# Kernel optimization log

Hardware: AMD Instinct MI355X
Metric: run time of the kernel (lower is better)

The kernel has to match this reference:

```python
import jax, jax.numpy as jnp
import numpy as np

B, N, M, K, H = 32, 2048, 16, 32, 2
EPS = 1e-7


def setup_inputs() -> dict:
    key = jax.random.key(0)
    k1, k2, k3, k4, k5 = jax.random.split(key, 5)
    coords = jax.random.normal(k1, (B, N, M), jnp.float32)
    hom = jax.random.randint(k2, (B, N), 0, H).astype(jnp.float32)
    # ragged lengths: valid points first, all-zero padding rows after
    lengths = jax.random.randint(k3, (B,), N // 2, N + 1)
    rowmask = (jnp.arange(N)[None, :] < lengths[:, None]).astype(jnp.float32)
    dgm = jnp.concatenate([hom[..., None], coords], axis=-1) * rowmask[..., None]
    # tf.random_normal_initializer default stddev = 0.05
    theta = 0.05 * jax.random.normal(k4, (K, M), jnp.float32)
    class_w = 0.05 * jax.random.normal(k5, (H,), jnp.float32)
    return {"dgm": dgm, "theta": theta, "class_w": class_w}


def reference(dgm, theta, class_w):
    # dgm: [B, N, M+1]; dgm[:,:,0] = homology class, rest = point coords
    b, n = dgm.shape[0], dgm.shape[1]
    k, m = theta.shape
    hom = jnp.clip(dgm[:, :, 0].astype(jnp.int32), 0, class_w.shape[0] - 1)  # [B,N]
    y = dgm[:, :, 1:]                                                        # [B,N,m]
    # while-loop semantics: process points until the FIRST all-zero row
    nonzero = jnp.any(dgm != 0, axis=-1)
    valid = jnp.cumprod(nonzero.astype(dgm.dtype), axis=1)                   # [B,N]
    w = class_w[hom] * valid                                                 # [B,N]
    # Poincare parametrization: z = theta_k * y, map R^m -> ball via z/(1+sqrt(1+|z|^2))
    z = y[:, None, :, :] * theta[None, :, None, :]                           # [B,K,N,m]
    zn2 = jnp.sum(z * z, axis=-1, keepdims=True)
    x = z / (1.0 + jnp.sqrt(1.0 + zn2))                                      # in unit ball
    # log map at origin (c=1): artanh(|x|) * x / |x|
    xn = jnp.sqrt(jnp.sum(x * x, axis=-1, keepdims=True))
    v = jnp.arctanh(jnp.minimum(xn, 1.0 - EPS)) * x / jnp.maximum(xn, EPS)   # [B,K,N,m]
    # per-(diagram, basis) class-weighted tangent sum
    T = jnp.einsum('bknm,bn->bkm', v, w)                                     # [B,K,m]
    # FAITHFUL to source: `sum` is never reset -> cumulative over (i, k) ordering
    S = jnp.cumsum(T.reshape(b * k, m), axis=0).reshape(b, k, m)
    # exp map at origin (c=1): tanh(|S|) * S / |S|
    sn = jnp.sqrt(jnp.sum(S * S, axis=-1, keepdims=True))
    xd = jnp.tanh(sn) * S / jnp.maximum(sn, EPS)
    yd = 2.0 * xd / (1.0 - jnp.sum(xd * xd, axis=-1, keepdims=True))
    return yd.reshape(b, k * m)
```

## Files before the change

kernel.cpp:

```cpp
#include <hip/hip_runtime.h>
#include <hip/hip_bf16.h>

constexpr int Bc = 32;
constexpr int Nc = 2048;
constexpr int Mc = 16;
constexpr int Kc = 32;
constexpr int ROWc = 17;
constexpr int CH = 256;
constexpr int NCH = Nc / CH;
constexpr float EPSc = 1e-7f;
constexpr float HALF_LN2 = 0.34657359028f;

__global__ __launch_bounds__(512) void k_T(const float* __restrict__ dgm,
                                           const float* __restrict__ theta,
                                           const float* __restrict__ class_w,
                                           float* __restrict__ P,
                                           int H) {
    __shared__ float stage[CH * 20];
    __shared__ float red[8 * 544];

    int bid = blockIdx.x;
    int b   = bid >> 3;
    int c   = bid & 7;
    int tid = threadIdx.x;
    int k   = tid & 31;
    int rg  = tid >> 5;

    const float4* src4 = (const float4*)(dgm + ((size_t)b * Nc + c * CH) * ROWc);
    for (int i = tid; i < (CH * ROWc) / 4; i += 512) {
        float4 v = src4[i];
        unsigned g = 4u * i;
#pragma unroll
        for (int e = 0; e < 4; ++e) {
            unsigned ge  = g + e;
            unsigned row = ge / 17u;
            unsigned col = ge - row * 17u;
            float val = (e == 0) ? v.x : (e == 1) ? v.y : (e == 2) ? v.z : v.w;
            stage[row * 20 + (col == 0 ? 0u : col + 3u)] = val;
        }
    }

    float th2[16];
    {
        const float4* t4 = (const float4*)theta;
#pragma unroll
        for (int q = 0; q < 4; ++q) {
            float4 tv = t4[k * 4 + q];
            th2[4*q+0] = tv.x * tv.x; th2[4*q+1] = tv.y * tv.y;
            th2[4*q+2] = tv.z * tv.z; th2[4*q+3] = tv.w * tv.w;
        }
    }
    float cw0 = class_w[0];
    float cw1 = (H > 1) ? class_w[1] : cw0;

    __syncthreads();

    float acc[16];
#pragma unroll
    for (int m = 0; m < 16; ++m) acc[m] = 0.0f;

#pragma unroll
    for (int j = 0; j < 16; ++j) {
        int row = rg * 16 + j;
        const float* rp = &stage[row * 20];
        float r0 = rp[0];
        float r[16];
        {
            float4* rv = (float4*)r;
            const float4* lp = (const float4*)(rp + 4);
            rv[0] = lp[0]; rv[1] = lp[1]; rv[2] = lp[2]; rv[3] = lp[3];
        }

        int h = (int)r0;
        h = max(0, min(h, H - 1));
        float wv = (H == 2) ? (h ? cw1 : cw0) : class_w[h];

        float za = 0.f, zb = 0.f, zc = 0.f, zd = 0.f;
#pragma unroll
        for (int m = 0; m < 16; m += 4) {
            za = fmaf(r[m]   * r[m],   th2[m],   za);
            zb = fmaf(r[m+1] * r[m+1], th2[m+1], zb);
            zc = fmaf(r[m+2] * r[m+2], th2[m+2], zc);
            zd = fmaf(r[m+3] * r[m+3], th2[m+3], zd);
        }
        float zn2 = (za + zb) + (zc + zd);
        float rs  = rsqrtf(fmaxf(zn2, 1e-30f));
        float zn  = zn2 * rs;
        float s   = sqrtf(1.0f + zn2);
        float at2 = __log2f(zn + s);
        float coef = HALF_LN2 * at2 * rs * wv;
#pragma unroll
        for (int m = 0; m < 16; ++m) acc[m] = fmaf(coef, r[m], acc[m]);
    }

#pragma unroll
    for (int m = 0; m < 16; ++m) acc[m] += __shfl_xor(acc[m], 32);

    int w = tid >> 6;
    if ((tid & 63) < 32) {
#pragma unroll
        for (int m = 0; m < 16; ++m) red[w * 544 + k * 17 + m] = acc[m];
    }
    __syncthreads();

    {
        int kk = tid >> 4;
        int mm = tid & 15;
        float s = 0.0f;
#pragma unroll
        for (int w2 = 0; w2 < 8; ++w2) s += red[w2 * 544 + kk * 17 + mm];
        P[(size_t)bid * 512 + tid] = s * theta[tid];
    }
}

__global__ __launch_bounds__(1024) void k_scan(const float* __restrict__ P,
                                               float* __restrict__ out) {
    __shared__ float buf[2][64][Mc];

    int tid = threadIdx.x;
    int m   = tid & 15;
    int seg = tid >> 4;

    float p[16];
    float run = 0.0f;
#pragma unroll
    for (int j = 0; j < 16; ++j) {
        int row = seg * 16 + j;
        int b   = row >> 5;
        int k   = row & 31;
        const float* q = P + (size_t)b * (NCH * 512) + k * 16 + m;
        float t0 = q[0]        + q[512]      + q[2 * 512] + q[3 * 512];
        float t1 = q[4 * 512]  + q[5 * 512]  + q[6 * 512] + q[7 * 512];
        run += t0 + t1;
        p[j] = run;
    }

    buf[0][seg][m] = run;
    __syncthreads();
    int src = 0;
#pragma unroll
    for (int d = 1; d < 64; d <<= 1) {
        float v = buf[src][seg][m];
        if (seg >= d) v += buf[src][seg - d][m];
        buf[src ^ 1][seg][m] = v;
        __syncthreads();
        src ^= 1;
    }
    float off = (seg > 0) ? buf[src][seg - 1][m] : 0.0f;

#pragma unroll
    for (int j = 0; j < 16; ++j) {
        float S = off + p[j];
        float sn2 = S * S;
        sn2 += __shfl_xor(sn2, 1);
        sn2 += __shfl_xor(sn2, 2);
        sn2 += __shfl_xor(sn2, 4);
        sn2 += __shfl_xor(sn2, 8);
        float sn = sqrtf(sn2);
        float e  = __expf(2.0f * sn);
        float t  = 1.0f - 2.0f / (e + 1.0f);
        float cc = t / fmaxf(sn, EPSc);
        float sx2 = cc * cc * sn2;
        float yd = 2.0f * cc * S / (1.0f - sx2);
        out[(size_t)(seg * 16 + j) * Mc + m] = yd;
    }
}

extern "C" void kernel_launch(void* const* d_in, const int* in_sizes, int n_in,
                              void* d_out, int out_size, void* d_ws, size_t ws_size,
                              hipStream_t stream) {
    const float* dgm     = (const float*)d_in[0];
    const float* theta   = (const float*)d_in[1];
    const float* class_w = (const float*)d_in[2];
    int H = in_sizes[2];

    float* P   = (float*)d_ws;
    float* out = (float*)d_out;

    k_T<<<Bc * NCH, 512, 0, stream>>>(dgm, theta, class_w, P, H);
    k_scan<<<1, 1024, 0, stream>>>(P, out);
}
```

Before: 32.87 us.

## Fuse partial-sum and scan kernels via last-block atomic counter

```diff
diff --git a/kernel.cpp b/kernel.cpp
--- a/kernel.cpp
+++ b/kernel.cpp
@@ -8,16 +8,20 @@
 constexpr int ROWc = 17;
 constexpr int CH = 256;
 constexpr int NCH = Nc / CH;
+constexpr int NBLK = Bc * NCH;
 constexpr float EPSc = 1e-7f;
 constexpr float HALF_LN2 = 0.34657359028f;
 
-__global__ __launch_bounds__(512) void k_T(const float* __restrict__ dgm,
-                                           const float* __restrict__ theta,
-                                           const float* __restrict__ class_w,
-                                           float* __restrict__ P,
-                                           int H) {
+__global__ __launch_bounds__(1024) void k_all(const float* __restrict__ dgm,
+                                              const float* __restrict__ theta,
+                                              const float* __restrict__ class_w,
+                                              float* __restrict__ P,
+                                              int* __restrict__ counter,
+                                              float* __restrict__ out,
+                                              int H) {
     __shared__ float stage[CH * 20];
-    __shared__ float red[8 * 544];
+    __shared__ float red[16 * 544];
+    __shared__ int   flag;
 
     int bid = blockIdx.x;
     int b   = bid >> 3;
@@ -27,7 +31,7 @@
     int rg  = tid >> 5;
 
     const float4* src4 = (const float4*)(dgm + ((size_t)b * Nc + c * CH) * ROWc);
-    for (int i = tid; i < (CH * ROWc) / 4; i += 512) {
+    for (int i = tid; i < (CH * ROWc) / 4; i += 1024) {
         float4 v = src4[i];
         unsigned g = 4u * i;
 #pragma unroll
@@ -60,8 +64,8 @@
     for (int m = 0; m < 16; ++m) acc[m] = 0.0f;
 
 #pragma unroll
-    for (int j = 0; j < 16; ++j) {
-        int row = rg * 16 + j;
+    for (int j = 0; j < 8; ++j) {
+        int row = rg * 8 + j;
         const float* rp = &stage[row * 20];
         float r0 = rp[0];
         float r[16];
@@ -103,21 +107,27 @@
     }
     __syncthreads();
 
-    {
+    if (tid < 512) {
         int kk = tid >> 4;
         int mm = tid & 15;
         float s = 0.0f;
 #pragma unroll
-        for (int w2 = 0; w2 < 8; ++w2) s += red[w2 * 544 + kk * 17 + mm];
+        for (int w2 = 0; w2 < 16; ++w2) s += red[w2 * 544 + kk * 17 + mm];
         P[(size_t)bid * 512 + tid] = s * theta[tid];
     }
-}
 
-__global__ __launch_bounds__(1024) void k_scan(const float* __restrict__ P,
-                                               float* __restrict__ out) {
-    __shared__ float buf[2][64][Mc];
+    __threadfence();
+    __syncthreads();
+    if (tid == 0) {
+        int old = atomicAdd(counter, 1);
+        flag = (old == NBLK - 1);
+    }
+    __syncthreads();
+    if (!flag) return;
+    __threadfence();
 
-    int tid = threadIdx.x;
+    float (*buf)[64][Mc] = (float (*)[64][Mc])red;
+
     int m   = tid & 15;
     int seg = tid >> 4;
 
@@ -126,11 +136,11 @@
 #pragma unroll
     for (int j = 0; j < 16; ++j) {
         int row = seg * 16 + j;
-        int b   = row >> 5;
-        int k   = row & 31;
-        const float* q = P + (size_t)b * (NCH * 512) + k * 16 + m;
-        float t0 = q[0]        + q[512]      + q[2 * 512] + q[3 * 512];
-        float t1 = q[4 * 512]  + q[5 * 512]  + q[6 * 512] + q[7 * 512];
+        int bb  = row >> 5;
+        int kk  = row & 31;
+        const float* q = P + (size_t)bb * (NCH * 512) + kk * 16 + m;
+        float t0 = q[0]       + q[512]     + q[2 * 512] + q[3 * 512];
+        float t1 = q[4 * 512] + q[5 * 512] + q[6 * 512] + q[7 * 512];
         run += t0 + t1;
         p[j] = run;
     }
@@ -174,9 +184,10 @@
     const float* class_w = (const float*)d_in[2];
     int H = in_sizes[2];
 
-    float* P   = (float*)d_ws;
-    float* out = (float*)d_out;
+    float* P       = (float*)d_ws;
+    int*   counter = (int*)((char*)d_ws + NBLK * 512 * sizeof(float));
+    float* out     = (float*)d_out;
 
-    k_T<<<Bc * NCH, 512, 0, stream>>>(dgm, theta, class_w, P, H);
-    k_scan<<<1, 1024, 0, stream>>>(P, out);
+    hipMemsetAsync(counter, 0, sizeof(int), stream);
+    k_all<<<NBLK, 1024, 0, stream>>>(dgm, theta, class_w, P, counter, out, H);
 }
```

After: 104.5 us. +217.8%, slower.

## Split basis dimension across blocks to raise grid parallelism in k_T

Applied to the files above, without the earlier changes.

```diff
diff --git a/kernel.cpp b/kernel.cpp
--- a/kernel.cpp
+++ b/kernel.cpp
@@ -8,6 +8,8 @@
 constexpr int ROWc = 17;
 constexpr int CH = 256;
 constexpr int NCH = Nc / CH;
+constexpr int KQ = 8;
+constexpr int NKQ = Kc / KQ;
 constexpr float EPSc = 1e-7f;
 constexpr float HALF_LN2 = 0.34657359028f;
 
@@ -17,14 +19,16 @@
                                            float* __restrict__ P,
                                            int H) {
     __shared__ float stage[CH * 20];
-    __shared__ float red[8 * 544];
+    __shared__ float red[8 * KQ * 17];
 
     int bid = blockIdx.x;
-    int b   = bid >> 3;
-    int c   = bid & 7;
+    int b   = bid >> 5;
+    int rem = bid & 31;
+    int kq  = rem >> 3;
+    int c   = rem & 7;
     int tid = threadIdx.x;
-    int k   = tid & 31;
-    int rg  = tid >> 5;
+    int k8  = tid & 7;
+    int rg  = tid >> 3;
 
     const float4* src4 = (const float4*)(dgm + ((size_t)b * Nc + c * CH) * ROWc);
     for (int i = tid; i < (CH * ROWc) / 4; i += 512) {
@@ -40,12 +44,13 @@
         }
     }
 
+    int kg = kq * KQ + k8;
     float th2[16];
     {
         const float4* t4 = (const float4*)theta;
 #pragma unroll
         for (int q = 0; q < 4; ++q) {
-            float4 tv = t4[k * 4 + q];
+            float4 tv = t4[kg * 4 + q];
             th2[4*q+0] = tv.x * tv.x; th2[4*q+1] = tv.y * tv.y;
             th2[4*q+2] = tv.z * tv.z; th2[4*q+3] = tv.w * tv.w;
         }
@@ -60,8 +65,8 @@
     for (int m = 0; m < 16; ++m) acc[m] = 0.0f;
 
 #pragma unroll
-    for (int j = 0; j < 16; ++j) {
-        int row = rg * 16 + j;
+    for (int j = 0; j < 4; ++j) {
+        int row = rg * 4 + j;
         const float* rp = &stage[row * 20];
         float r0 = rp[0];
         float r[16];
@@ -94,22 +99,26 @@
     }
 
 #pragma unroll
-    for (int m = 0; m < 16; ++m) acc[m] += __shfl_xor(acc[m], 32);
+    for (int m = 0; m < 16; ++m) {
+        acc[m] += __shfl_xor(acc[m], 8);
+        acc[m] += __shfl_xor(acc[m], 16);
+        acc[m] += __shfl_xor(acc[m], 32);
+    }
 
     int w = tid >> 6;
-    if ((tid & 63) < 32) {
+    if ((tid & 63) < 8) {
 #pragma unroll
-        for (int m = 0; m < 16; ++m) red[w * 544 + k * 17 + m] = acc[m];
+        for (int m = 0; m < 16; ++m) red[w * (KQ * 17) + k8 * 17 + m] = acc[m];
     }
     __syncthreads();
 
-    {
+    if (tid < KQ * 16) {
         int kk = tid >> 4;
         int mm = tid & 15;
         float s = 0.0f;
 #pragma unroll
-        for (int w2 = 0; w2 < 8; ++w2) s += red[w2 * 544 + kk * 17 + mm];
-        P[(size_t)bid * 512 + tid] = s * theta[tid];
+        for (int w2 = 0; w2 < 8; ++w2) s += red[w2 * (KQ * 17) + kk * 17 + mm];
+        P[(size_t)bid * 128 + tid] = s * theta[kq * 128 + tid];
     }
 }
 
@@ -128,9 +137,11 @@
         int row = seg * 16 + j;
         int b   = row >> 5;
         int k   = row & 31;
-        const float* q = P + (size_t)b * (NCH * 512) + k * 16 + m;
-        float t0 = q[0]        + q[512]      + q[2 * 512] + q[3 * 512];
-        float t1 = q[4 * 512]  + q[5 * 512]  + q[6 * 512] + q[7 * 512];
+        int kq  = k >> 3;
+        int k8  = k & 7;
+        const float* q = P + (size_t)b * 4096 + kq * 1024 + k8 * 16 + m;
+        float t0 = q[0]       + q[128]     + q[2 * 128] + q[3 * 128];
+        float t1 = q[4 * 128] + q[5 * 128] + q[6 * 128] + q[7 * 128];
         run += t0 + t1;
         p[j] = run;
     }
@@ -177,6 +188,6 @@
     float* P   = (float*)d_ws;
     float* out = (float*)d_out;
 
-    k_T<<<Bc * NCH, 512, 0, stream>>>(dgm, theta, class_w, P, H);
+    k_T<<<Bc * NKQ * NCH, 512, 0, stream>>>(dgm, theta, class_w, P, H);
     k_scan<<<1, 1024, 0, stream>>>(P, out);
 }
```

Measured after the change: 31.20 us. 1.05x faster.
